# Kernel optimization log

Measured on AMD Instinct MI355X. Metric: run time of the kernel, lower is better.

## Reference

```python
import jax, jax.numpy as jnp
import numpy as np
from jax import lax

EPS = 1e-5
NUM_CLASSES = 133


def conv2d(x, w, stride, pad, b=None):
    # x: [N,C,H,W], w: [O,I,kh,kw]
    out = lax.conv_general_dilated(x, w, (stride, stride), ((pad, pad), (pad, pad)),
                                   dimension_numbers=('NCHW', 'OIHW', 'NCHW'))
    if b is not None:
        out = out + b[None, :, None, None]
    return out


def cbn(x, y, embed_w, C):
    # ConditionalBatchNorm2d in training mode: batch stats (biased var), affine from embedding
    mean = x.mean(axis=(0, 2, 3), keepdims=True)
    var = x.var(axis=(0, 2, 3), keepdims=True)
    xn = (x - mean) * lax.rsqrt(var + EPS)
    gb = embed_w[y]                      # [O, 2C]
    gamma, beta = gb[:, :C], gb[:, C:]
    return gamma[:, :, None, None] * xn + beta[:, :, None, None]


def lrelu(x):
    return jnp.where(x >= 0, x, 0.2 * x)


def clstm_layer(x_seq, w, b, hidden_dim):
    # x_seq: [T, B, Cin, 16, 16] -> (all h: [T,B,hid,16,16], last h: [B,hid,16,16])
    B = x_seq.shape[1]
    h0 = jnp.zeros((B, hidden_dim, 16, 16), x_seq.dtype)

    def step(carry, x):
        h, c = carry
        cc = conv2d(jnp.concatenate([x, h], axis=1), w, 1, 2, b)  # k=5, pad=2
        i, f, o, g = jnp.split(cc, 4, axis=1)
        c = jax.nn.sigmoid(f) * c + jax.nn.sigmoid(i) * jnp.tanh(g)
        h = jax.nn.sigmoid(o) * jnp.tanh(c)
        return (h, c), h

    (h, _), hs = lax.scan(step, (h0, h0), x_seq)
    return hs, h


def setup_inputs() -> dict:
    key = jax.random.key(0)
    ks = jax.random.split(key, 24)
    O, C_in, H = 8, 512, 254
    B, T = 4, 2
    d = {}
    d['h'] = jax.random.normal(ks[0], (O, C_in, H, H), jnp.float32)
    d['objs'] = jax.random.randint(ks[1], (O,), 0, NUM_CLASSES)
    d['obj_to_img'] = jnp.repeat(jnp.arange(B), T)  # sorted, equal-sized groups

    def w(k, shape):
        fan_in = shape[1] * shape[2] * shape[3]
        return jax.random.normal(k, shape, jnp.float32) / np.sqrt(fan_in)

    def embed(k, C):
        g = 1.0 + 0.02 * jax.random.normal(k, (NUM_CLASSES, C), jnp.float32)
        return jnp.concatenate([g, jnp.zeros((NUM_CLASSES, C), jnp.float32)], axis=1)

    d['c1_w'] = w(ks[2], (32, 512, 1, 1))
    d['c2_w'] = w(ks[3], (64, 32, 4, 4))
    d['c3_w'] = w(ks[4], (128, 64, 4, 4))
    d['c4_w'] = w(ks[5], (256, 128, 4, 4))
    d['c5_w'] = w(ks[6], (512, 256, 4, 4))
    d['e1'] = embed(ks[7], 32)
    d['e2'] = embed(ks[8], 64)
    d['e3'] = embed(ks[9], 128)
    d['e4'] = embed(ks[10], 256)
    d['e5'] = embed(ks[11], 512)
    # ConvLSTM layers: hidden [128, 64, 64], kernel 5x5, input_dim 512
    d['lw0'] = w(ks[12], (4 * 128, 512 + 128, 5, 5))
    d['lb0'] = jnp.zeros((4 * 128,), jnp.float32)
    d['lw1'] = w(ks[13], (4 * 64, 128 + 64, 5, 5))
    d['lb1'] = jnp.zeros((4 * 64,), jnp.float32)
    d['lw2'] = w(ks[14], (4 * 64, 64 + 64, 5, 5))
    d['lb2'] = jnp.zeros((4 * 64,), jnp.float32)
    return d


def reference(objs, obj_to_img, h, c1_w, c2_w, c3_w, c4_w, c5_w,
              e1, e2, e3, e4, e5, lw0, lb0, lw1, lb1, lw2, lb2):
    x = lrelu(cbn(conv2d(h, c1_w, 1, 1), objs, e1, 32))    # [O,32,256,256]
    x = lrelu(cbn(conv2d(x, c2_w, 2, 1), objs, e2, 64))    # [O,64,128,128]
    x = lrelu(cbn(conv2d(x, c3_w, 2, 1), objs, e3, 128))   # [O,128,64,64]
    x = cbn(conv2d(x, c4_w, 2, 1), objs, e4, 256)          # no activation after bn4 (as in source)
    x = cbn(conv2d(x, c5_w, 2, 1), objs, e5, 512)          # [O,512,16,16], no activation after bn5

    # Group ragged per-image object sequences. The torch loop groups consecutive
    # equal obj_to_img ids; with equal group sizes this is a static reshape.
    o2i = np.asarray(obj_to_img)
    B = int(o2i.max()) + 1
    O = x.shape[0]
    T = O // B
    assert B * T == O, 'reference assumes equal-sized, sorted object groups'
    seq = x.reshape(B, T, 512, 16, 16).transpose(1, 0, 2, 3, 4)  # [T,B,512,16,16]

    hs, _ = clstm_layer(seq, lw0, lb0, 128)
    hs, _ = clstm_layer(hs, lw1, lb1, 64)
    _, h_last = clstm_layer(hs, lw2, lb2, 64)
    return h_last  # [B,64,16,16]
```

## Files before the change

### kernel.cpp

```cpp
#include <hip/hip_runtime.h>
#include <math.h>

#define LEAK 0.2f

typedef __attribute__((ext_vector_type(8))) short bf16x8;
typedef __attribute__((ext_vector_type(4))) float f32x4;

__device__ __forceinline__ unsigned short f2bf(float f) {
  unsigned u = __float_as_uint(f);
  u += 0x7FFFu + ((u >> 16) & 1u);
  return (unsigned short)(u >> 16);
}
__device__ __forceinline__ unsigned pack2(float a, float b) {
  return (unsigned)f2bf(a) | ((unsigned)f2bf(b) << 16);
}

#define MFMA16(a, b, c) __builtin_amdgcn_mfma_f32_16x16x32_bf16(a, b, c, 0, 0, 0)

__device__ __forceinline__ void wprep_std(
    const float* __restrict__ w, unsigned short* __restrict__ dst,
    int O, int C, int TAPS, int i)
{
  int o = i / (C * TAPS);
  int r = i - o * C * TAPS;
  int c = r / TAPS, tap = r - c * TAPS;
  dst[((size_t)tap * O + o) * C + c] = f2bf(w[i]);
}

__global__ __launch_bounds__(256) void wprepAll_kernel(
    const float* c1w, const float* c2w, const float* c3w, const float* c4w,
    const float* c5w, const float* lw0, const float* lw1, const float* lw2,
    unsigned short* wb1, unsigned short* wb2, unsigned short* wb3,
    unsigned short* wb4, unsigned short* wb5, unsigned short* wbf0,
    unsigned short* wbf1, unsigned short* wbf2)
{
  int i = blockIdx.x * 256 + threadIdx.x;
  if (i < 16384) {
    int o = i >> 9, c = i & 511;
    wb1[(((c >> 5) * 32) + o) * 32 + (c & 31)] = f2bf(c1w[i]);
    return;
  }
  i -= 16384;
  if (i < 32768)   { wprep_std(c2w, wb2, 64, 32, 16, i);    return; }
  i -= 32768;
  if (i < 131072)  { wprep_std(c3w, wb3, 128, 64, 16, i);   return; }
  i -= 131072;
  if (i < 524288)  { wprep_std(c4w, wb4, 256, 128, 16, i);  return; }
  i -= 524288;
  if (i < 2097152) { wprep_std(c5w, wb5, 512, 256, 16, i);  return; }
  i -= 2097152;
  if (i < 8192000) { wprep_std(lw0, wbf0, 512, 640, 25, i); return; }
  i -= 8192000;
  if (i < 1228800) { wprep_std(lw1, wbf1, 256, 192, 25, i); return; }
  i -= 1228800;
  if (i < 819200)  { wprep_std(lw2, wbf2, 256, 128, 25, i); return; }
}

__global__ __launch_bounds__(256) void conv1M_kernel(
    const float* __restrict__ h, const unsigned short* __restrict__ wbc,
    float* __restrict__ xT, float* __restrict__ part1)
{
  __shared__ __align__(16) unsigned short inT[512 * 40];
  __shared__ float red1[4][4][2][4][2];

  const int n = blockIdx.y;
  const int px0 = blockIdx.x * 512;
  const int tid = threadIdx.x, lane = tid & 63, wid = tid >> 6;
  const int ln15 = lane & 15, kg = lane >> 4;

  f32x4 acc[2][8];
#pragma unroll
  for (int m = 0; m < 2; ++m)
#pragma unroll
    for (int f = 0; f < 8; ++f) acc[m][f] = (f32x4){0.f, 0.f, 0.f, 0.f};

  for (int kc = 0; kc < 16; ++kc) {
    __syncthreads();
#pragma unroll
    for (int k = 0; k < 8; ++k) {
      const int u = tid + k * 256;
      const int chp = u >> 7;
      const int pxq = u & 127;
      const int ch = 2 * chp;
      const int pxl = 4 * pxq;
      const int pxg = px0 + pxl;
      const int r = pxg >> 8;
      const int c0 = pxg & 255;
      const bool rint = (r >= 1 && r <= 254);
      const float* hrow0 = h + ((size_t)(n * 512 + kc * 32 + ch)) * 64516
                             + (size_t)(r - 1) * 254 + (c0 - 1);
      const float* hrow1 = hrow0 + 64516;
      float v0[4], v1[4];
#pragma unroll
      for (int j = 0; j < 4; ++j) {
        const int c = c0 + j;
        const bool ok = rint && (c >= 1) && (c <= 254);
        v0[j] = ok ? hrow0[j] : 0.f;
        v1[j] = ok ? hrow1[j] : 0.f;
      }
      const int chs = ch ^ ((pxq & 3) << 3);
#pragma unroll
      for (int j = 0; j < 4; ++j)
        *(unsigned*)&inT[(pxl + j) * 40 + chs] = pack2(v0[j], v1[j]);
    }
    __syncthreads();

    const bf16x8 a0 = *(const bf16x8*)(wbc + ((size_t)(kc * 32 + ln15)) * 32 + kg * 8);
    const bf16x8 a1 = *(const bf16x8*)(wbc + ((size_t)(kc * 32 + 16 + ln15)) * 32 + kg * 8);
#pragma unroll
    for (int f = 0; f < 8; ++f) {
      const int pxr = wid * 128 + f * 16 + ln15;
      const int chs = (kg * 8) ^ (((pxr >> 2) & 3) << 3);
      const bf16x8 b = *(const bf16x8*)&inT[pxr * 40 + chs];
      acc[0][f] = MFMA16(a0, b, acc[0][f]);
      acc[1][f] = MFMA16(a1, b, acc[1][f]);
    }
  }

#pragma unroll
  for (int mf = 0; mf < 2; ++mf) {
#pragma unroll
    for (int f = 0; f < 8; ++f) {
      const int px = px0 + wid * 128 + f * 16 + ln15;
      const int o = mf * 16 + kg * 4;
      *(f32x4*)(xT + ((size_t)n * 65536 + px) * 32 + o) = acc[mf][f];
    }
  }

#pragma unroll
  for (int mf = 0; mf < 2; ++mf) {
#pragma unroll
    for (int j = 0; j < 4; ++j) {
      float s = 0.f, q = 0.f;
#pragma unroll
      for (int f = 0; f < 8; ++f) { float v = acc[mf][f][j]; s += v; q += v * v; }
#pragma unroll
      for (int mk = 1; mk < 16; mk <<= 1) {
        s += __shfl_xor(s, mk);
        q += __shfl_xor(q, mk);
      }
      if (ln15 == 0) { red1[wid][kg][mf][j][0] = s; red1[wid][kg][mf][j][1] = q; }
    }
  }
  __syncthreads();
  if (tid < 32) {
    const int mf = tid >> 4, kgi = (tid >> 2) & 3, j = tid & 3;
    float s = red1[0][kgi][mf][j][0] + red1[1][kgi][mf][j][0]
            + red1[2][kgi][mf][j][0] + red1[3][kgi][mf][j][0];
    float q = red1[0][kgi][mf][j][1] + red1[1][kgi][mf][j][1]
            + red1[2][kgi][mf][j][1] + red1[3][kgi][mf][j][1];
    atomicAdd(&part1[tid], s);
    atomicAdd(&part1[32 + tid], q);
  }
}

__global__ __launch_bounds__(256) void cbn1T_kernel(
    const float* __restrict__ xT, const float* __restrict__ part1, float invN,
    const float* __restrict__ e1, const int* __restrict__ objs,
    unsigned short* __restrict__ T2)
{
  __shared__ float st[32][4];
  const int n = blockIdx.y;
  if (threadIdx.x < 32) {
    int y = objs[n];
    float s = part1[threadIdx.x], q = part1[32 + threadIdx.x];
    float mean = s * invN;
    st[threadIdx.x][0] = mean;
    st[threadIdx.x][1] = rsqrtf(q * invN - mean * mean + 1e-5f);
    st[threadIdx.x][2] = e1[(size_t)y * 64 + threadIdx.x];
    st[threadIdx.x][3] = e1[(size_t)y * 64 + 32 + threadIdx.x];
  }
  __syncthreads();
  const int pix = blockIdx.x * 256 + threadIdx.x;
  const int r = pix >> 8, c = pix & 255;
  const float* src = xT + ((size_t)n * 65536 + pix) * 32;
  unsigned short* dst = T2 + ((size_t)n * 66564 + (size_t)(r + 1) * 258 + (c + 1)) * 32;
  unsigned outw[16];
#pragma unroll
  for (int q = 0; q < 8; ++q) {
    float4 t = ((const float4*)src)[q];
    float v[4] = {t.x, t.y, t.z, t.w};
#pragma unroll
    for (int j = 0; j < 4; ++j) {
      int ch = q * 4 + j;
      float z = (v[j] - st[ch][0]) * st[ch][1] * st[ch][2] + st[ch][3];
      v[j] = z >= 0.f ? z : LEAK * z;
    }
    outw[2 * q]     = pack2(v[0], v[1]);
    outw[2 * q + 1] = pack2(v[2], v[3]);
  }
  uint4* d4 = (uint4*)dst;
#pragma unroll
  for (int q = 0; q < 4; ++q)
    d4[q] = make_uint4(outw[4*q], outw[4*q+1], outw[4*q+2], outw[4*q+3]);
}

template <int C, int O, int H>
__global__ __launch_bounds__(256) void conv4T_kernel(
    const unsigned short* __restrict__ Tin, const unsigned short* __restrict__ wb,
    float* __restrict__ raw, float* __restrict__ part)
{
  constexpr int HIN2 = 2 * H + 2;
  constexpr int KC = C / 32;
  constexpr int LOGH = (H == 128 ? 7 : (H == 64 ? 6 : (H == 32 ? 5 : 4)));
  __shared__ float red[4][4][2][4][2];
  const int o0 = blockIdx.x * 64;
  const int strip = blockIdx.y;
  const int n = blockIdx.z;
  const int tid = threadIdx.x, lane = tid & 63, wid = tid >> 6;
  const int wm = wid >> 1, wn = wid & 1;
  const int ln15 = lane & 15, kg = lane >> 4;
  const unsigned short* inb = Tin + (size_t)n * (HIN2 * HIN2) * C;

  f32x4 acc[2][2];
#pragma unroll
  for (int m = 0; m < 2; ++m)
#pragma unroll
    for (int nt = 0; nt < 2; ++nt) acc[m][nt] = (f32x4){0.f, 0.f, 0.f, 0.f};

  const int gp0 = strip * 64 + (wn * 2 + 0) * 16;
  const int gp1 = strip * 64 + (wn * 2 + 1) * 16;
  const int r_0 = gp0 >> LOGH, c_0 = (gp0 & (H - 1)) + ln15;
  const int r_1 = gp1 >> LOGH, c_1 = (gp1 & (H - 1)) + ln15;

  for (int kc = 0; kc < KC; ++kc) {
    const int cb = kc * 32 + kg * 8;
#pragma unroll
    for (int tap = 0; tap < 16; ++tap) {
      const int ky = tap >> 2, kx = tap & 3;
      const unsigned short* ap = wb + ((size_t)tap * O + o0 + wm * 32 + ln15) * C + cb;
      bf16x8 a0 = *(const bf16x8*)ap;
      bf16x8 a1 = *(const bf16x8*)(ap + (size_t)16 * C);
      bf16x8 b0 = *(const bf16x8*)(inb + (size_t)((2 * r_0 + ky) * HIN2 + 2 * c_0 + kx) * C + cb);
      bf16x8 b1 = *(const bf16x8*)(inb + (size_t)((2 * r_1 + ky) * HIN2 + 2 * c_1 + kx) * C + cb);
      acc[0][0] = MFMA16(a0, b0, acc[0][0]);
      acc[1][0] = MFMA16(a1, b0, acc[1][0]);
      acc[0][1] = MFMA16(a0, b1, acc[0][1]);
      acc[1][1] = MFMA16(a1, b1, acc[1][1]);
    }
  }

#pragma unroll
  for (int mf = 0; mf < 2; ++mf) {
    const int o = o0 + wm * 32 + mf * 16 + kg * 4;
#pragma unroll
    for (int nt = 0; nt < 2; ++nt) {
      const int gp = strip * 64 + (wn * 2 + nt) * 16 + ln15;
      *(f32x4*)(raw + ((size_t)n * (H * H) + gp) * O + o) = acc[mf][nt];
    }
  }

#pragma unroll
  for (int mf = 0; mf < 2; ++mf) {
#pragma unroll
    for (int j = 0; j < 4; ++j) {
      float v0 = acc[mf][0][j], v1 = acc[mf][1][j];
      float s = v0 + v1, q = v0 * v0 + v1 * v1;
#pragma unroll
      for (int mk = 1; mk < 16; mk <<= 1) {
        s += __shfl_xor(s, mk);
        q += __shfl_xor(q, mk);
      }
      if (ln15 == 0) { red[wid][kg][mf][j][0] = s; red[wid][kg][mf][j][1] = q; }
    }
  }
  __syncthreads();
  if (tid < 64) {
    const int wmi = tid >> 5, mf = (tid >> 4) & 1, kgi = (tid >> 2) & 3, j = tid & 3;
    float s = red[wmi * 2][kgi][mf][j][0] + red[wmi * 2 + 1][kgi][mf][j][0];
    float q = red[wmi * 2][kgi][mf][j][1] + red[wmi * 2 + 1][kgi][mf][j][1];
    atomicAdd(&part[o0 + tid], s);
    atomicAdd(&part[O + o0 + tid], q);
  }
}

template <int C, int H, int P2, int CSO, bool LRELU, bool LMAP>
__global__ __launch_bounds__(256) void cbnT_kernel(
    const float* __restrict__ raw, const float* __restrict__ part, float invN,
    const float* __restrict__ embed, const int* __restrict__ objs,
    unsigned short* __restrict__ Tout)
{
  constexpr int W2 = H + 2 * P2;
  constexpr int LOGH = (H == 128 ? 7 : (H == 64 ? 6 : (H == 32 ? 5 : 4)));
  const int n = blockIdx.y;
  const int y = objs[n];
  const int pix = blockIdx.x * 64 + (threadIdx.x >> 2);
  const int r = pix >> LOGH, c = pix & (H - 1);
  const float* src = raw + ((size_t)n * (H * H) + pix) * C;
  const size_t nb = LMAP ? (size_t)((n & 1) * 4 + (n >> 1)) * (W2 * W2) * CSO
                         : (size_t)n * (W2 * W2) * CSO;
  unsigned short* dst = Tout + nb + ((size_t)(r + P2) * W2 + c + P2) * CSO;
  const float* gam = embed + (size_t)y * 2 * C;
  const float* bet = gam + C;
  for (int cs = (threadIdx.x & 3); cs < C / 8; cs += 4) {
    float4 ps0 = ((const float4*)part)[cs * 2],       ps1 = ((const float4*)part)[cs * 2 + 1];
    float4 pq0 = ((const float4*)(part + C))[cs * 2], pq1 = ((const float4*)(part + C))[cs * 2 + 1];
    float4 g0 = ((const float4*)gam)[cs * 2], g1 = ((const float4*)gam)[cs * 2 + 1];
    float4 b0 = ((const float4*)bet)[cs * 2], b1 = ((const float4*)bet)[cs * 2 + 1];
    float4 v0 = ((const float4*)src)[cs * 2], v1 = ((const float4*)src)[cs * 2 + 1];
    float sv[8] = {ps0.x, ps0.y, ps0.z, ps0.w, ps1.x, ps1.y, ps1.z, ps1.w};
    float qv[8] = {pq0.x, pq0.y, pq0.z, pq0.w, pq1.x, pq1.y, pq1.z, pq1.w};
    float gv[8] = {g0.x, g0.y, g0.z, g0.w, g1.x, g1.y, g1.z, g1.w};
    float bv[8] = {b0.x, b0.y, b0.z, b0.w, b1.x, b1.y, b1.z, b1.w};
    float vv[8] = {v0.x, v0.y, v0.z, v0.w, v1.x, v1.y, v1.z, v1.w};
    float o_[8];
#pragma unroll
    for (int k = 0; k < 8; ++k) {
      float m = sv[k] * invN;
      float rs = rsqrtf(qv[k] * invN - m * m + 1e-5f);
      float z = (vv[k] - m) * rs * gv[k] + bv[k];
      o_[k] = (LRELU && z < 0.f) ? LEAK * z : z;
    }
    ((uint4*)dst)[cs] = make_uint4(pack2(o_[0], o_[1]), pack2(o_[2], o_[3]),
                                   pack2(o_[4], o_[5]), pack2(o_[6], o_[7]));
  }
}

template <int O, int C, int CS, int WM, int WN, int NCHUNK>
__global__ __launch_bounds__(256) void conv5L_kernel(
    const unsigned short* __restrict__ Lin, const unsigned short* __restrict__ wbf,
    float* __restrict__ pp)
{
  constexpr int FN = 16 / WN;
  const int o0 = blockIdx.x * (WM * 32);
  const int b = blockIdx.y, ks = blockIdx.z;
  const int tid = threadIdx.x, lane = tid & 63, wid = tid >> 6;
  const int wm = wid / WN, wn = wid % WN;
  const int ln15 = lane & 15, kg = lane >> 4;
  const unsigned short* inb = Lin + (size_t)b * 400 * CS;

  f32x4 acc[2][FN];
#pragma unroll
  for (int m = 0; m < 2; ++m)
#pragma unroll
    for (int nt = 0; nt < FN; ++nt) acc[m][nt] = (f32x4){0.f, 0.f, 0.f, 0.f};

  for (int kc = 0; kc < NCHUNK; ++kc) {
    const int cb = (ks * NCHUNK + kc) * 32 + kg * 8;
    for (int tap = 0; tap < 25; ++tap) {
      const int ty = tap / 5, tx = tap - 5 * ty;
      const unsigned short* ap = wbf + ((size_t)tap * O + o0 + wm * 32 + ln15) * C + cb;
      bf16x8 a0 = *(const bf16x8*)ap;
      bf16x8 a1 = *(const bf16x8*)(ap + (size_t)16 * C);
#pragma unroll
      for (int nt = 0; nt < FN; ++nt) {
        const int p = (wn * FN + nt) * 16 + ln15;
        const int prow = p >> 4, pcol = p & 15;
        bf16x8 bfv = *(const bf16x8*)(inb + (size_t)((prow + ty) * 20 + pcol + tx) * CS + cb);
        acc[0][nt] = MFMA16(a0, bfv, acc[0][nt]);
        acc[1][nt] = MFMA16(a1, bfv, acc[1][nt]);
      }
    }
  }

#pragma unroll
  for (int mf = 0; mf < 2; ++mf) {
    const int o = o0 + wm * 32 + mf * 16 + kg * 4;
#pragma unroll
    for (int nt = 0; nt < FN; ++nt) {
      const int pix = (wn * FN + nt) * 16 + ln15;
      *(f32x4*)(pp + (((size_t)(ks * 4 + b)) * 256 + pix) * O + o) = acc[mf][nt];
    }
  }
}

template <int Hc, int CS, int CX, int CSN>
__global__ __launch_bounds__(256) void lstm_pointT_kernel(
    const float* __restrict__ pp, int KS, const float* __restrict__ bias,
    float* __restrict__ cT, unsigned short* __restrict__ own,
    unsigned short* __restrict__ nxt, float* __restrict__ fout)
{
  constexpr int C4 = Hc / 4;
  constexpr int O = 4 * Hc;
  constexpr int LOGC4 = (C4 == 32 ? 5 : 4);
  const int i = blockIdx.x * 256 + threadIdx.x;
  const int c4 = i & (C4 - 1);
  const int pix = (i >> LOGC4) & 255;
  const int b = i >> (LOGC4 + 8);

  float g[4][4];
#pragma unroll
  for (int gt = 0; gt < 4; ++gt)
#pragma unroll
    for (int j = 0; j < 4; ++j) g[gt][j] = 0.f;

  for (int ks = 0; ks < KS; ++ks) {
    const float* base = pp + (((size_t)(ks * 4 + b)) * 256 + pix) * O + c4 * 4;
#pragma unroll
    for (int gt = 0; gt < 4; ++gt) {
      float4 v = *(const float4*)(base + gt * Hc);
      g[gt][0] += v.x; g[gt][1] += v.y; g[gt][2] += v.z; g[gt][3] += v.w;
    }
  }
#pragma unroll
  for (int gt = 0; gt < 4; ++gt) {
    float4 bv = *(const float4*)(bias + gt * Hc + c4 * 4);
    g[gt][0] += bv.x; g[gt][1] += bv.y; g[gt][2] += bv.z; g[gt][3] += bv.w;
  }

  float* cp = cT + ((size_t)b * 256 + pix) * Hc + c4 * 4;
  float4 cold = *(const float4*)cp;
  float co[4] = {cold.x, cold.y, cold.z, cold.w};
  float hn[4];
#pragma unroll
  for (int j = 0; j < 4; ++j) {
    float si = 1.f / (1.f + expf(-g[0][j]));
    float sf = 1.f / (1.f + expf(-g[1][j]));
    float so = 1.f / (1.f + expf(-g[2][j]));
    float cn = sf * co[j] + si * tanhf(g[3][j]);
    co[j] = cn;
    hn[j] = so * tanhf(cn);
  }
  *(float4*)cp = make_float4(co[0], co[1], co[2], co[3]);

  const int prow = pix >> 4, pcol = pix & 15;
  const int ppix = (prow + 2) * 20 + pcol + 2;
  uint2 hb = make_uint2(pack2(hn[0], hn[1]), pack2(hn[2], hn[3]));
  if (own) *(uint2*)(own + ((size_t)b * 400 + ppix) * CS + CX + c4 * 4) = hb;
  if (nxt) *(uint2*)(nxt + ((size_t)b * 400 + ppix) * CSN + c4 * 4) = hb;
  if (fout) {
#pragma unroll
    for (int j = 0; j < 4; ++j)
      fout[((size_t)b * Hc + c4 * 4 + j) * 256 + pix] = hn[j];
  }
}

extern "C" void kernel_launch(void* const* d_in, const int* in_sizes, int n_in,
                              void* d_out, int out_size, void* d_ws, size_t ws_size,
                              hipStream_t stream)
{
  const float* h    = (const float*)d_in[0];
  const int*   objs = (const int*)  d_in[1];
  const float* c1w  = (const float*)d_in[3];
  const float* c2w  = (const float*)d_in[4];
  const float* c3w  = (const float*)d_in[5];
  const float* c4w  = (const float*)d_in[6];
  const float* c5w  = (const float*)d_in[7];
  const float* e1   = (const float*)d_in[8];
  const float* e2   = (const float*)d_in[9];
  const float* e3   = (const float*)d_in[10];
  const float* e4   = (const float*)d_in[11];
  const float* e5   = (const float*)d_in[12];
  const float* lw0  = (const float*)d_in[13];
  const float* lb0  = (const float*)d_in[14];
  const float* lw1  = (const float*)d_in[15];
  const float* lb1  = (const float*)d_in[16];
  const float* lw2  = (const float*)d_in[17];
  const float* lb2  = (const float*)d_in[18];

  char* p = (char*)d_ws;
  auto alloc = [&](size_t bytes) { char* r = p; p += (bytes + 255) & ~(size_t)255; return r; };
  float* x1T  = (float*)alloc((size_t)8 * 65536 * 32 * 4);
  float* raw2 = (float*)alloc((size_t)8 * 16384 * 64 * 4);
  float* raw3 = (float*)alloc((size_t)8 * 4096 * 128 * 4);
  float* raw4 = (float*)alloc((size_t)8 * 1024 * 256 * 4);
  float* raw5 = (float*)alloc((size_t)8 * 256 * 512 * 4);
  float* pp   = (float*)alloc((size_t)10 * 4 * 256 * 512 * 4);
  unsigned short* wb1  = (unsigned short*)alloc((size_t)32 * 512 * 2);
  unsigned short* wb2  = (unsigned short*)alloc((size_t)16 * 64 * 32 * 2);
  unsigned short* wb3  = (unsigned short*)alloc((size_t)16 * 128 * 64 * 2);
  unsigned short* wb4  = (unsigned short*)alloc((size_t)16 * 256 * 128 * 2);
  unsigned short* wb5  = (unsigned short*)alloc((size_t)16 * 512 * 256 * 2);
  unsigned short* wbf0 = (unsigned short*)alloc((size_t)25 * 512 * 640 * 2);
  unsigned short* wbf1 = (unsigned short*)alloc((size_t)25 * 256 * 192 * 2);
  unsigned short* wbf2 = (unsigned short*)alloc((size_t)25 * 256 * 128 * 2);
  char* zbase = p;
  unsigned short* T2 = (unsigned short*)alloc((size_t)8 * 66564 * 32 * 2);
  unsigned short* T3 = (unsigned short*)alloc((size_t)8 * 16900 * 64 * 2);
  unsigned short* T4 = (unsigned short*)alloc((size_t)8 * 4356 * 128 * 2);
  unsigned short* T5 = (unsigned short*)alloc((size_t)8 * 1156 * 256 * 2);
  unsigned short* L0in = (unsigned short*)alloc((size_t)2 * 4 * 400 * 640 * 2);
  unsigned short* L1in = (unsigned short*)alloc((size_t)2 * 4 * 400 * 192 * 2);
  unsigned short* L2in = (unsigned short*)alloc((size_t)2 * 4 * 400 * 128 * 2);
  float* cT0 = (float*)alloc((size_t)4 * 256 * 128 * 4);
  float* cT1 = (float*)alloc((size_t)4 * 256 * 64 * 4);
  float* cT2 = (float*)alloc((size_t)4 * 256 * 64 * 4);
  float* part1 = (float*)alloc(2 * 32 * 4);
  float* part2 = (float*)alloc(2 * 64 * 4);
  float* part3 = (float*)alloc(2 * 128 * 4);
  float* part4 = (float*)alloc(2 * 256 * 4);
  float* part5 = (float*)alloc(2 * 512 * 4);
  size_t zsize = (size_t)(p - zbase);

  hipMemsetAsync(zbase, 0, zsize, stream);
  wprepAll_kernel<<<(13041664 + 255) / 256, 256, 0, stream>>>(
      c1w, c2w, c3w, c4w, c5w, lw0, lw1, lw2,
      wb1, wb2, wb3, wb4, wb5, wbf0, wbf1, wbf2);

  conv1M_kernel<<<dim3(128, 8), 256, 0, stream>>>(h, wb1, x1T, part1);
  cbn1T_kernel<<<dim3(256, 8), 256, 0, stream>>>(x1T, part1, 1.f / (float)(8 * 65536), e1, objs, T2);

  conv4T_kernel<32, 64, 128><<<dim3(1, 256, 8), 256, 0, stream>>>(T2, wb2, raw2, part2);
  cbnT_kernel<64, 128, 1, 64, true, false><<<dim3(256, 8), 256, 0, stream>>>(
      raw2, part2, 1.f / (float)(8 * 16384), e2, objs, T3);

  conv4T_kernel<64, 128, 64><<<dim3(2, 64, 8), 256, 0, stream>>>(T3, wb3, raw3, part3);
  cbnT_kernel<128, 64, 1, 128, true, false><<<dim3(64, 8), 256, 0, stream>>>(
      raw3, part3, 1.f / (float)(8 * 4096), e3, objs, T4);

  conv4T_kernel<128, 256, 32><<<dim3(4, 16, 8), 256, 0, stream>>>(T4, wb4, raw4, part4);
  cbnT_kernel<256, 32, 1, 256, false, false><<<dim3(16, 8), 256, 0, stream>>>(
      raw4, part4, 1.f / (float)(8 * 1024), e4, objs, T5);

  conv4T_kernel<256, 512, 16><<<dim3(8, 4, 8), 256, 0, stream>>>(T5, wb5, raw5, part5);
  cbnT_kernel<512, 16, 2, 640, false, true><<<dim3(4, 8), 256, 0, stream>>>(
      raw5, part5, 1.f / (float)(8 * 256), e5, objs, L0in);

  for (int t = 0; t < 2; ++t) {
    conv5L_kernel<512, 640, 640, 2, 2, 2><<<dim3(8, 4, 10), 256, 0, stream>>>(
        L0in + (size_t)t * 4 * 400 * 640, wbf0, pp);
    lstm_pointT_kernel<128, 640, 512, 192><<<128, 256, 0, stream>>>(
        pp, 10, lb0, cT0,
        (t == 0) ? L0in + (size_t)4 * 400 * 640 : nullptr,
        L1in + (size_t)t * 4 * 400 * 192, nullptr);
  }

  for (int t = 0; t < 2; ++t) {
    conv5L_kernel<256, 192, 192, 1, 4, 1><<<dim3(8, 4, 6), 256, 0, stream>>>(
        L1in + (size_t)t * 4 * 400 * 192, wbf1, pp);
    lstm_pointT_kernel<64, 192, 128, 128><<<64, 256, 0, stream>>>(
        pp, 6, lb1, cT1,
        (t == 0) ? L1in + (size_t)4 * 400 * 192 : nullptr,
        L2in + (size_t)t * 4 * 400 * 128, nullptr);
  }

  for (int t = 0; t < 2; ++t) {
    conv5L_kernel<256, 128, 128, 1, 4, 1><<<dim3(8, 4, 4), 256, 0, stream>>>(
        L2in + (size_t)t * 4 * 400 * 128, wbf2, pp);
    lstm_pointT_kernel<64, 128, 64, 1><<<64, 256, 0, stream>>>(
        pp, 4, lb2, cT2,
        (t == 0) ? L2in + (size_t)4 * 400 * 128 : nullptr,
        nullptr, (t == 1) ? (float*)d_out : nullptr);
  }
}
```

Before: 1.128 ms.

## Double-buffer conv1 staging, retile conv4 blocks, precompute LSTM input convs for both steps

Conv1 now handles one image row per block and double-buffers the LDS input tile, so loading the next channel chunk overlaps the MFMAs on the current one. Conv4 gains a WM template parameter so the deeper layers use narrower output tiles and launch more blocks. The LSTM conv5L kernel is restructured to compute the input-channel contributions for both timesteps in one launch, split per 32-channel chunk. Only the recurrent hidden-state chunks are convolved at step two, which takes input work off the serial chain. This needs a larger partial-sum buffer, and the pointwise kernel has to reduce more slices.

```diff
diff --git a/kernel.cpp b/kernel.cpp
--- a/kernel.cpp
+++ b/kernel.cpp
@@ -60,68 +60,69 @@
     const float* __restrict__ h, const unsigned short* __restrict__ wbc,
     float* __restrict__ xT, float* __restrict__ part1)
 {
-  __shared__ __align__(16) unsigned short inT[512 * 40];
+  __shared__ __align__(16) unsigned short inT[2][256 * 40];
   __shared__ float red1[4][4][2][4][2];
 
-  const int n = blockIdx.y;
-  const int px0 = blockIdx.x * 512;
+  const int n = blockIdx.y, r = blockIdx.x;
+  const int px0 = r * 256;
   const int tid = threadIdx.x, lane = tid & 63, wid = tid >> 6;
   const int ln15 = lane & 15, kg = lane >> 4;
-
-  f32x4 acc[2][8];
+  const bool rint = (r >= 1 && r <= 254);
+
+  f32x4 acc[2][4];
 #pragma unroll
   for (int m = 0; m < 2; ++m)
 #pragma unroll
-    for (int f = 0; f < 8; ++f) acc[m][f] = (f32x4){0.f, 0.f, 0.f, 0.f};
-
+    for (int f = 0; f < 4; ++f) acc[m][f] = (f32x4){0.f, 0.f, 0.f, 0.f};
+
+#define STAGE1(KC, BUF)                                                          \
+  {                                                                              \
+    _Pragma("unroll")                                                            \
+    for (int k = 0; k < 4; ++k) {                                                \
+      const int ch = 2 * (k * 4 + wid);                                          \
+      const int c0 = 4 * lane;                                                   \
+      const float* p0 = h + ((size_t)(n * 512 + (KC) * 32 + ch)) * 64516         \
+                          + (size_t)(r - 1) * 254 + (c0 - 1);                    \
+      const float* p1 = p0 + 64516;                                              \
+      float v0[4], v1[4];                                                        \
+      _Pragma("unroll")                                                          \
+      for (int j = 0; j < 4; ++j) {                                              \
+        const int c = c0 + j;                                                    \
+        const bool ok = rint && (c >= 1) && (c <= 254);                          \
+        v0[j] = ok ? p0[j] : 0.f;                                                \
+        v1[j] = ok ? p1[j] : 0.f;                                                \
+      }                                                                          \
+      const int chs = ch ^ ((lane & 3) << 3);                                    \
+      _Pragma("unroll")                                                          \
+      for (int j = 0; j < 4; ++j)                                                \
+        *(unsigned*)&inT[BUF][(c0 + j) * 40 + chs] = pack2(v0[j], v1[j]);        \
+    }                                                                            \
+  }
+
+  STAGE1(0, 0);
+  __syncthreads();
   for (int kc = 0; kc < 16; ++kc) {
-    __syncthreads();
-#pragma unroll
-    for (int k = 0; k < 8; ++k) {
-      const int u = tid + k * 256;
-      const int chp = u >> 7;
-      const int pxq = u & 127;
-      const int ch = 2 * chp;
-      const int pxl = 4 * pxq;
-      const int pxg = px0 + pxl;
-      const int r = pxg >> 8;
-      const int c0 = pxg & 255;
-      const bool rint = (r >= 1 && r <= 254);
-      const float* hrow0 = h + ((size_t)(n * 512 + kc * 32 + ch)) * 64516
-                             + (size_t)(r - 1) * 254 + (c0 - 1);
-      const float* hrow1 = hrow0 + 64516;
-      float v0[4], v1[4];
-#pragma unroll
-      for (int j = 0; j < 4; ++j) {
-        const int c = c0 + j;
-        const bool ok = rint && (c >= 1) && (c <= 254);
-        v0[j] = ok ? hrow0[j] : 0.f;
-        v1[j] = ok ? hrow1[j] : 0.f;
-      }
-      const int chs = ch ^ ((pxq & 3) << 3);
-#pragma unroll
-      for (int j = 0; j < 4; ++j)
-        *(unsigned*)&inT[(pxl + j) * 40 + chs] = pack2(v0[j], v1[j]);
-    }
-    __syncthreads();
-
+    if (kc < 15) STAGE1(kc + 1, (kc + 1) & 1);
     const bf16x8 a0 = *(const bf16x8*)(wbc + ((size_t)(kc * 32 + ln15)) * 32 + kg * 8);
     const bf16x8 a1 = *(const bf16x8*)(wbc + ((size_t)(kc * 32 + 16 + ln15)) * 32 + kg * 8);
-#pragma unroll
-    for (int f = 0; f < 8; ++f) {
-      const int pxr = wid * 128 + f * 16 + ln15;
+    const int cur = kc & 1;
+#pragma unroll
+    for (int f = 0; f < 4; ++f) {
+      const int pxr = wid * 64 + f * 16 + ln15;
       const int chs = (kg * 8) ^ (((pxr >> 2) & 3) << 3);
-      const bf16x8 b = *(const bf16x8*)&inT[pxr * 40 + chs];
+      const bf16x8 b = *(const bf16x8*)&inT[cur][pxr * 40 + chs];
       acc[0][f] = MFMA16(a0, b, acc[0][f]);
       acc[1][f] = MFMA16(a1, b, acc[1][f]);
     }
-  }
+    __syncthreads();
+  }
+#undef STAGE1
 
 #pragma unroll
   for (int mf = 0; mf < 2; ++mf) {
 #pragma unroll
-    for (int f = 0; f < 8; ++f) {
-      const int px = px0 + wid * 128 + f * 16 + ln15;
+    for (int f = 0; f < 4; ++f) {
+      const int px = px0 + wid * 64 + f * 16 + ln15;
       const int o = mf * 16 + kg * 4;
       *(f32x4*)(xT + ((size_t)n * 65536 + px) * 32 + o) = acc[mf][f];
     }
@@ -133,7 +134,7 @@
     for (int j = 0; j < 4; ++j) {
       float s = 0.f, q = 0.f;
 #pragma unroll
-      for (int f = 0; f < 8; ++f) { float v = acc[mf][f][j]; s += v; q += v * v; }
+      for (int f = 0; f < 4; ++f) { float v = acc[mf][f][j]; s += v; q += v * v; }
 #pragma unroll
       for (int mk = 1; mk < 16; mk <<= 1) {
         s += __shfl_xor(s, mk);
@@ -195,33 +196,38 @@
     d4[q] = make_uint4(outw[4*q], outw[4*q+1], outw[4*q+2], outw[4*q+3]);
 }
 
-template <int C, int O, int H>
+template <int C, int O, int H, int WM>
 __global__ __launch_bounds__(256) void conv4T_kernel(
     const unsigned short* __restrict__ Tin, const unsigned short* __restrict__ wb,
     float* __restrict__ raw, float* __restrict__ part)
 {
   constexpr int HIN2 = 2 * H + 2;
   constexpr int KC = C / 32;
+  constexpr int WN4 = 4 / WM;
+  constexpr int NT = WM;
   constexpr int LOGH = (H == 128 ? 7 : (H == 64 ? 6 : (H == 32 ? 5 : 4)));
   __shared__ float red[4][4][2][4][2];
-  const int o0 = blockIdx.x * 64;
+  const int o0 = blockIdx.x * (WM * 32);
   const int strip = blockIdx.y;
   const int n = blockIdx.z;
   const int tid = threadIdx.x, lane = tid & 63, wid = tid >> 6;
-  const int wm = wid >> 1, wn = wid & 1;
+  const int wm = wid / WN4, wn = wid % WN4;
   const int ln15 = lane & 15, kg = lane >> 4;
   const unsigned short* inb = Tin + (size_t)n * (HIN2 * HIN2) * C;
 
-  f32x4 acc[2][2];
+  f32x4 acc[2][NT];
 #pragma unroll
   for (int m = 0; m < 2; ++m)
 #pragma unroll
-    for (int nt = 0; nt < 2; ++nt) acc[m][nt] = (f32x4){0.f, 0.f, 0.f, 0.f};
-
-  const int gp0 = strip * 64 + (wn * 2 + 0) * 16;
-  const int gp1 = strip * 64 + (wn * 2 + 1) * 16;
-  const int r_0 = gp0 >> LOGH, c_0 = (gp0 & (H - 1)) + ln15;
-  const int r_1 = gp1 >> LOGH, c_1 = (gp1 & (H - 1)) + ln15;
+    for (int nt = 0; nt < NT; ++nt) acc[m][nt] = (f32x4){0.f, 0.f, 0.f, 0.f};
+
+  int r_[NT], c_[NT];
+#pragma unroll
+  for (int nt = 0; nt < NT; ++nt) {
+    const int gp = strip * 64 + (wn * NT + nt) * 16;
+    r_[nt] = gp >> LOGH;
+    c_[nt] = (gp & (H - 1)) + ln15;
+  }
 
   for (int kc = 0; kc < KC; ++kc) {
     const int cb = kc * 32 + kg * 8;
@@ -231,12 +237,12 @@
       const unsigned short* ap = wb + ((size_t)tap * O + o0 + wm * 32 + ln15) * C + cb;
       bf16x8 a0 = *(const bf16x8*)ap;
       bf16x8 a1 = *(const bf16x8*)(ap + (size_t)16 * C);
-      bf16x8 b0 = *(const bf16x8*)(inb + (size_t)((2 * r_0 + ky) * HIN2 + 2 * c_0 + kx) * C + cb);
-      bf16x8 b1 = *(const bf16x8*)(inb + (size_t)((2 * r_1 + ky) * HIN2 + 2 * c_1 + kx) * C + cb);
-      acc[0][0] = MFMA16(a0, b0, acc[0][0]);
-      acc[1][0] = MFMA16(a1, b0, acc[1][0]);
-      acc[0][1] = MFMA16(a0, b1, acc[0][1]);
-      acc[1][1] = MFMA16(a1, b1, acc[1][1]);
+#pragma unroll
+      for (int nt = 0; nt < NT; ++nt) {
+        bf16x8 b = *(const bf16x8*)(inb + (size_t)((2 * r_[nt] + ky) * HIN2 + 2 * c_[nt] + kx) * C + cb);
+        acc[0][nt] = MFMA16(a0, b, acc[0][nt]);
+        acc[1][nt] = MFMA16(a1, b, acc[1][nt]);
+      }
     }
   }
 
@@ -244,8 +250,8 @@
   for (int mf = 0; mf < 2; ++mf) {
     const int o = o0 + wm * 32 + mf * 16 + kg * 4;
 #pragma unroll
-    for (int nt = 0; nt < 2; ++nt) {
-      const int gp = strip * 64 + (wn * 2 + nt) * 16 + ln15;
+    for (int nt = 0; nt < NT; ++nt) {
+      const int gp = strip * 64 + (wn * NT + nt) * 16 + ln15;
       *(f32x4*)(raw + ((size_t)n * (H * H) + gp) * O + o) = acc[mf][nt];
     }
   }
@@ -254,8 +260,9 @@
   for (int mf = 0; mf < 2; ++mf) {
 #pragma unroll
     for (int j = 0; j < 4; ++j) {
-      float v0 = acc[mf][0][j], v1 = acc[mf][1][j];
-      float s = v0 + v1, q = v0 * v0 + v1 * v1;
+      float s = 0.f, q = 0.f;
+#pragma unroll
+      for (int nt = 0; nt < NT; ++nt) { float v = acc[mf][nt][j]; s += v; q += v * v; }
 #pragma unroll
       for (int mk = 1; mk < 16; mk <<= 1) {
         s += __shfl_xor(s, mk);
@@ -265,10 +272,14 @@
     }
   }
   __syncthreads();
-  if (tid < 64) {
+  if (tid < WM * 32) {
     const int wmi = tid >> 5, mf = (tid >> 4) & 1, kgi = (tid >> 2) & 3, j = tid & 3;
-    float s = red[wmi * 2][kgi][mf][j][0] + red[wmi * 2 + 1][kgi][mf][j][0];
-    float q = red[wmi * 2][kgi][mf][j][1] + red[wmi * 2 + 1][kgi][mf][j][1];
+    float s = 0.f, q = 0.f;
+#pragma unroll
+    for (int w = 0; w < WN4; ++w) {
+      s += red[wmi * WN4 + w][kgi][mf][j][0];
+      q += red[wmi * WN4 + w][kgi][mf][j][1];
+    }
     atomicAdd(&part[o0 + tid], s);
     atomicAdd(&part[O + o0 + tid], q);
   }
@@ -316,18 +327,20 @@
   }
 }
 
-template <int O, int C, int CS, int WM, int WN, int NCHUNK>
+template <int O, int CS, int WM, int WN>
 __global__ __launch_bounds__(256) void conv5L_kernel(
     const unsigned short* __restrict__ Lin, const unsigned short* __restrict__ wbf,
-    float* __restrict__ pp)
+    float* __restrict__ pp, int kbeg, int slot0, size_t lin_tstr, size_t pp_tstr)
 {
   constexpr int FN = 16 / WN;
   const int o0 = blockIdx.x * (WM * 32);
-  const int b = blockIdx.y, ks = blockIdx.z;
+  const int b = blockIdx.y & 3, t = blockIdx.y >> 2;
+  const int ks = blockIdx.z;
   const int tid = threadIdx.x, lane = tid & 63, wid = tid >> 6;
   const int wm = wid / WN, wn = wid % WN;
   const int ln15 = lane & 15, kg = lane >> 4;
-  const unsigned short* inb = Lin + (size_t)b * 400 * CS;
+  const unsigned short* inb = Lin + (size_t)t * lin_tstr + (size_t)b * 400 * CS;
+  float* ppb = pp + (size_t)t * pp_tstr + ((size_t)(slot0 + ks) * 4 + b) * (256 * O);
 
   f32x4 acc[2][FN];
 #pragma unroll
@@ -335,21 +348,19 @@
 #pragma unroll
     for (int nt = 0; nt < FN; ++nt) acc[m][nt] = (f32x4){0.f, 0.f, 0.f, 0.f};
 
-  for (int kc = 0; kc < NCHUNK; ++kc) {
-    const int cb = (ks * NCHUNK + kc) * 32 + kg * 8;
-    for (int tap = 0; tap < 25; ++tap) {
-      const int ty = tap / 5, tx = tap - 5 * ty;
-      const unsigned short* ap = wbf + ((size_t)tap * O + o0 + wm * 32 + ln15) * C + cb;
-      bf16x8 a0 = *(const bf16x8*)ap;
-      bf16x8 a1 = *(const bf16x8*)(ap + (size_t)16 * C);
-#pragma unroll
-      for (int nt = 0; nt < FN; ++nt) {
-        const int p = (wn * FN + nt) * 16 + ln15;
-        const int prow = p >> 4, pcol = p & 15;
-        bf16x8 bfv = *(const bf16x8*)(inb + (size_t)((prow + ty) * 20 + pcol + tx) * CS + cb);
-        acc[0][nt] = MFMA16(a0, bfv, acc[0][nt]);
-        acc[1][nt] = MFMA16(a1, bfv, acc[1][nt]);
-      }
+  const int cb = (kbeg + ks) * 32 + kg * 8;
+  for (int tap = 0; tap < 25; ++tap) {
+    const int ty = tap / 5, tx = tap - 5 * ty;
+    const unsigned short* ap = wbf + ((size_t)tap * O + o0 + wm * 32 + ln15) * CS + cb;
+    bf16x8 a0 = *(const bf16x8*)ap;
+    bf16x8 a1 = *(const bf16x8*)(ap + (size_t)16 * CS);
+#pragma unroll
+    for (int nt = 0; nt < FN; ++nt) {
+      const int p = (wn * FN + nt) * 16 + ln15;
+      const int prow = p >> 4, pcol = p & 15;
+      bf16x8 bfv = *(const bf16x8*)(inb + (size_t)((prow + ty) * 20 + pcol + tx) * CS + cb);
+      acc[0][nt] = MFMA16(a0, bfv, acc[0][nt]);
+      acc[1][nt] = MFMA16(a1, bfv, acc[1][nt]);
     }
   }
 
@@ -359,7 +370,7 @@
 #pragma unroll
     for (int nt = 0; nt < FN; ++nt) {
       const int pix = (wn * FN + nt) * 16 + ln15;
-      *(f32x4*)(pp + (((size_t)(ks * 4 + b)) * 256 + pix) * O + o) = acc[mf][nt];
+      *(f32x4*)(ppb + (size_t)pix * O + o) = acc[mf][nt];
     }
   }
 }
@@ -455,7 +466,7 @@
   float* raw3 = (float*)alloc((size_t)8 * 4096 * 128 * 4);
   float* raw4 = (float*)alloc((size_t)8 * 1024 * 256 * 4);
   float* raw5 = (float*)alloc((size_t)8 * 256 * 512 * 4);
-  float* pp   = (float*)alloc((size_t)10 * 4 * 256 * 512 * 4);
+  float* pp   = (float*)alloc((size_t)2 * 20 * 4 * 256 * 512 * 4);
   unsigned short* wb1  = (unsigned short*)alloc((size_t)32 * 512 * 2);
   unsigned short* wb2  = (unsigned short*)alloc((size_t)16 * 64 * 32 * 2);
   unsigned short* wb3  = (unsigned short*)alloc((size_t)16 * 128 * 64 * 2);
@@ -487,49 +498,61 @@
       c1w, c2w, c3w, c4w, c5w, lw0, lw1, lw2,
       wb1, wb2, wb3, wb4, wb5, wbf0, wbf1, wbf2);
 
-  conv1M_kernel<<<dim3(128, 8), 256, 0, stream>>>(h, wb1, x1T, part1);
+  conv1M_kernel<<<dim3(256, 8), 256, 0, stream>>>(h, wb1, x1T, part1);
   cbn1T_kernel<<<dim3(256, 8), 256, 0, stream>>>(x1T, part1, 1.f / (float)(8 * 65536), e1, objs, T2);
 
-  conv4T_kernel<32, 64, 128><<<dim3(1, 256, 8), 256, 0, stream>>>(T2, wb2, raw2, part2);
+  conv4T_kernel<32, 64, 128, 2><<<dim3(1, 256, 8), 256, 0, stream>>>(T2, wb2, raw2, part2);
   cbnT_kernel<64, 128, 1, 64, true, false><<<dim3(256, 8), 256, 0, stream>>>(
       raw2, part2, 1.f / (float)(8 * 16384), e2, objs, T3);
 
-  conv4T_kernel<64, 128, 64><<<dim3(2, 64, 8), 256, 0, stream>>>(T3, wb3, raw3, part3);
+  conv4T_kernel<64, 128, 64, 2><<<dim3(2, 64, 8), 256, 0, stream>>>(T3, wb3, raw3, part3);
   cbnT_kernel<128, 64, 1, 128, true, false><<<dim3(64, 8), 256, 0, stream>>>(
       raw3, part3, 1.f / (float)(8 * 4096), e3, objs, T4);
 
-  conv4T_kernel<128, 256, 32><<<dim3(4, 16, 8), 256, 0, stream>>>(T4, wb4, raw4, part4);
+  conv4T_kernel<128, 256, 32, 1><<<dim3(8, 16, 8), 256, 0, stream>>>(T4, wb4, raw4, part4);
   cbnT_kernel<256, 32, 1, 256, false, false><<<dim3(16, 8), 256, 0, stream>>>(
       raw4, part4, 1.f / (float)(8 * 1024), e4, objs, T5);
 
-  conv4T_kernel<256, 512, 16><<<dim3(8, 4, 8), 256, 0, stream>>>(T5, wb5, raw5, part5);
+  conv4T_kernel<256, 512, 16, 1><<<dim3(16, 4, 8), 256, 0, stream>>>(T5, wb5, raw5, part5);
   cbnT_kernel<512, 16, 2, 640, false, true><<<dim3(4, 8), 256, 0, stream>>>(
       raw5, part5, 1.f / (float)(8 * 256), e5, objs, L0in);
 
-  for (int t = 0; t < 2; ++t) {
-    conv5L_kernel<512, 640, 640, 2, 2, 2><<<dim3(8, 4, 10), 256, 0, stream>>>(
-        L0in + (size_t)t * 4 * 400 * 640, wbf0, pp);
+  {
+    const size_t LINT = (size_t)4 * 400 * 640;
+    const size_t PPT  = (size_t)20 * 4 * 256 * 512;
+    conv5L_kernel<512, 640, 2, 2><<<dim3(8, 8, 16), 256, 0, stream>>>(
+        L0in, wbf0, pp, 0, 0, LINT, PPT);
     lstm_pointT_kernel<128, 640, 512, 192><<<128, 256, 0, stream>>>(
-        pp, 10, lb0, cT0,
-        (t == 0) ? L0in + (size_t)4 * 400 * 640 : nullptr,
-        L1in + (size_t)t * 4 * 400 * 192, nullptr);
-  }
-
-  for (int t = 0; t < 2; ++t) {
-    conv5L_kernel<256, 192, 192, 1, 4, 1><<<dim3(8, 4, 6), 256, 0, stream>>>(
-        L1in + (size_t)t * 4 * 400 * 192, wbf1, pp);
+        pp, 16, lb0, cT0, L0in + LINT, L1in, nullptr);
+    conv5L_kernel<512, 640, 2, 2><<<dim3(8, 4, 4), 256, 0, stream>>>(
+        L0in + LINT, wbf0, pp + PPT, 16, 16, 0, 0);
+    lstm_pointT_kernel<128, 640, 512, 192><<<128, 256, 0, stream>>>(
+        pp + PPT, 20, lb0, cT0, nullptr, L1in + (size_t)4 * 400 * 192, nullptr);
+  }
+
+  {
+    const size_t LINT = (size_t)4 * 400 * 192;
+    const size_t PPT  = (size_t)6 * 4 * 256 * 256;
+    conv5L_kernel<256, 192, 1, 4><<<dim3(8, 8, 4), 256, 0, stream>>>(
+        L1in, wbf1, pp, 0, 0, LINT, PPT);
     lstm_pointT_kernel<64, 192, 128, 128><<<64, 256, 0, stream>>>(
-        pp, 6, lb1, cT1,
-        (t == 0) ? L1in + (size_t)4 * 400 * 192 : nullptr,
-        L2in + (size_t)t * 4 * 400 * 128, nullptr);
-  }
-
-  for (int t = 0; t < 2; ++t) {
-    conv5L_kernel<256, 128, 128, 1, 4, 1><<<dim3(8, 4, 4), 256, 0, stream>>>(
-        L2in + (size_t)t * 4 * 400 * 128, wbf2, pp);
+        pp, 4, lb1, cT1, L1in + LINT, L2in, nullptr);
+    conv5L_kernel<256, 192, 1, 4><<<dim3(8, 4, 2), 256, 0, stream>>>(
+        L1in + LINT, wbf1, pp + PPT, 4, 4, 0, 0);
+    lstm_pointT_kernel<64, 192, 128, 128><<<64, 256, 0, stream>>>(
+        pp + PPT, 6, lb1, cT1, nullptr, L2in + (size_t)4 * 400 * 128, nullptr);
+  }
+
+  {
+    const size_t LINT = (size_t)4 * 400 * 128;
+    const size_t PPT  = (size_t)4 * 4 * 256 * 256;
+    conv5L_kernel<256, 128, 1, 4><<<dim3(8, 8, 2), 256, 0, stream>>>(
+        L2in, wbf2, pp, 0, 0, LINT, PPT);
     lstm_pointT_kernel<64, 128, 64, 1><<<64, 256, 0, stream>>>(
-        pp, 4, lb2, cT2,
-        (t == 0) ? L2in + (size_t)4 * 400 * 128 : nullptr,
-        nullptr, (t == 1) ? (float*)d_out : nullptr);
-  }
-}
+        pp, 2, lb2, cT2, L2in + LINT, nullptr, nullptr);
+    conv5L_kernel<256, 128, 1, 4><<<dim3(8, 4, 2), 256, 0, stream>>>(
+        L2in + LINT, wbf2, pp + PPT, 2, 2, 0, 0);
+    lstm_pointT_kernel<64, 128, 64, 1><<<64, 256, 0, stream>>>(
+        pp + PPT, 4, lb2, cT2, nullptr, nullptr, (float*)d_out);
+  }
+}
```

Result: faster. 1.095 ms (-2.9%).
